# Optimization experiments

Hardware: AMD Instinct MI355X
Metric: run time of the kernel (lower is better)

## Reference

```python
import jax, jax.numpy as jnp
import numpy as np

B, S, D = 2, 2048, 768
H = 12
HD = D // H  # head_dim = 64
WINDOW = 128
NEG = -1e9


def setup_inputs() -> dict:
    key = jax.random.key(0)
    k1, k2, k3 = jax.random.split(key, 3)
    x = jax.random.normal(k1, (B, S, D), dtype=jnp.float32)
    padding_mask = jnp.ones((B, S), dtype=jnp.float32)
    Wqkv = jax.random.normal(k2, (D, 3 * D), dtype=jnp.float32) * (1.0 / np.sqrt(D))
    Wo = jax.random.normal(k3, (D, D), dtype=jnp.float32) * (1.0 / np.sqrt(D))
    return {"x": x, "padding_mask": padding_mask, "Wqkv": Wqkv, "Wo": Wo}


def reference(x, padding_mask, Wqkv, Wo):
    b, s = x.shape[0], x.shape[1]
    qkv = x @ Wqkv  # [b, s, 3D]
    qkv = qkv.reshape(b, s, 3, H, HD)
    q = qkv[:, :, 0]  # [b, s, H, HD]
    k = qkv[:, :, 1]
    v = qkv[:, :, 2]
    # scores: [b, H, s, s]
    scores = jnp.einsum("bqhd,bkhd->bhqk", q, k) / jnp.sqrt(jnp.asarray(HD, x.dtype))
    # sliding-window additive mask
    idx = jnp.arange(s)
    sw_mask = (jnp.abs(idx[:, None] - idx[None, :]) <= WINDOW // 2).astype(jnp.float32)
    scores = scores + (1.0 - sw_mask)[None, None, :, :] * NEG
    # padding mask over keys
    scores = scores + (1.0 - padding_mask)[:, None, None, :] * NEG
    attn = jax.nn.softmax(scores, axis=-1)
    out = jnp.einsum("bhqk,bkhd->bqhd", attn, v).reshape(b, s, D)
    return out @ Wo
```

## Files before the change

### kernel.cpp

```cpp
#include <hip/hip_runtime.h>
#include <stdint.h>

typedef short bf16x8 __attribute__((ext_vector_type(8)));
typedef float f32x4 __attribute__((ext_vector_type(4)));

#define SEQ_ 2048
#define DM_ 768
#define NH_ 12

__device__ __forceinline__ unsigned short f2bf(float f) {
  unsigned int u = __float_as_uint(f);
  u += 0x7fffu + ((u >> 16) & 1u);
  return (unsigned short)(u >> 16);
}

__device__ __forceinline__ void load_lds16(const unsigned short* g, unsigned short* l) {
  __builtin_amdgcn_global_load_lds((__attribute__((address_space(1))) void*)g,
                                   (__attribute__((address_space(3))) void*)l, 16, 0, 0);
}

__device__ __forceinline__ void transpose_body(const float* __restrict__ src,
                                               unsigned short* __restrict__ dst,
                                               int R, int C, int bx, int by,
                                               float (*t)[65]) {
  int c0 = bx << 6, r0 = by << 6;
  int tid = threadIdx.x;
#pragma unroll
  for (int i = 0; i < 4; i++) {
    int e = (i * 256 + tid) * 4;
    int r = e >> 6, c = e & 63;
    float4 v = *(const float4*)(src + (size_t)(r0 + r) * C + c0 + c);
    t[r][c] = v.x; t[r][c + 1] = v.y; t[r][c + 2] = v.z; t[r][c + 3] = v.w;
  }
  __syncthreads();
#pragma unroll
  for (int i = 0; i < 4; i++) {
    int e = (i * 256 + tid) * 4;
    int r = e >> 6, c = e & 63;
    unsigned short o4[4];
#pragma unroll
    for (int j = 0; j < 4; j++) o4[j] = f2bf(t[c + j][r]);
    *(uint2*)(dst + (size_t)(c0 + r) * R + r0 + c) = *(const uint2*)o4;
  }
}

__global__ __launch_bounds__(256) void prep(const float* __restrict__ x,
                                            const float* __restrict__ Wqkv,
                                            const float* __restrict__ Wo,
                                            unsigned short* __restrict__ xb,
                                            unsigned short* __restrict__ wqkvt,
                                            unsigned short* __restrict__ wot) {
  __shared__ float t[64][65];
  int blk = blockIdx.x;
  if (blk < 3072) {
    int i = (blk * 256 + threadIdx.x) * 4;
    float4 v = *(const float4*)(x + i);
    unsigned short o[4] = {f2bf(v.x), f2bf(v.y), f2bf(v.z), f2bf(v.w)};
    *(uint2*)(xb + i) = *(const uint2*)o;
  } else if (blk < 3072 + 432) {
    int idx = blk - 3072;
    transpose_body(Wqkv, wqkvt, DM_, 3 * DM_, idx % 36, idx / 36, t);
  } else {
    int idx = blk - 3504;
    transpose_body(Wo, wot, DM_, DM_, idx % 12, idx / 12, t);
  }
}

__device__ __forceinline__ void gemm_mainloop(const unsigned short* __restrict__ A,
                                              const unsigned short* __restrict__ Bt,
                                              int m0, int n0,
                                              unsigned short* As, unsigned short* Bs,
                                              f32x4 acc[4][4]) {
  const int K = 768;
  int tid = threadIdx.x, wv = tid >> 6, ln = tid & 63, quad = ln >> 4, lrow = ln & 15;
  const unsigned short* a0 = A + (size_t)(m0 + (tid >> 2)) * K + (tid & 3) * 8;
  const unsigned short* a1 = a0 + (size_t)64 * K;
  const unsigned short* b0 = Bt + (size_t)(n0 + (tid >> 2)) * K + (tid & 3) * 8;
  const unsigned short* b1 = b0 + (size_t)64 * K;
  int mw = (wv >> 1) << 6, nw = (wv & 1) << 6;
  for (int kt = 0; kt < K; kt += 32) {
    load_lds16(a0 + kt, As + tid * 8);
    load_lds16(a1 + kt, As + (256 + tid) * 8);
    load_lds16(b0 + kt, Bs + tid * 8);
    load_lds16(b1 + kt, Bs + (256 + tid) * 8);
    __syncthreads();
    bf16x8 af[4], bfr[4];
#pragma unroll
    for (int i = 0; i < 4; i++)
      af[i] = *(const bf16x8*)(As + (mw + i * 16 + lrow) * 32 + quad * 8);
#pragma unroll
    for (int j = 0; j < 4; j++)
      bfr[j] = *(const bf16x8*)(Bs + (nw + j * 16 + lrow) * 32 + quad * 8);
#pragma unroll
    for (int i = 0; i < 4; i++)
#pragma unroll
      for (int j = 0; j < 4; j++)
        acc[i][j] = __builtin_amdgcn_mfma_f32_16x16x32_bf16(af[i], bfr[j], acc[i][j], 0, 0, 0);
    __syncthreads();
  }
}

__global__ __launch_bounds__(256, 3) void gemm_qkv(const unsigned short* __restrict__ A,
                                                   const unsigned short* __restrict__ Bt,
                                                   unsigned short* __restrict__ Qb,
                                                   unsigned short* __restrict__ Kb,
                                                   unsigned short* __restrict__ Vtb) {
  __shared__ unsigned short smem[2 * 128 * 32];
  unsigned short* As = smem;
  unsigned short* Bs = smem + 128 * 32;
  f32x4 acc[4][4];
  f32x4 z = {0.f, 0.f, 0.f, 0.f};
#pragma unroll
  for (int i = 0; i < 4; i++)
#pragma unroll
    for (int j = 0; j < 4; j++) acc[i][j] = z;
  int m0 = blockIdx.x << 7, n0 = blockIdx.y << 7;
  gemm_mainloop(A, Bt, m0, n0, As, Bs, acc);
  int tid = threadIdx.x, wv = tid >> 6, ln = tid & 63, quad = ln >> 4, lrow = ln & 15;
  int mw_l = (wv >> 1) << 6, nw_l = (wv & 1) << 6;
  int bb = m0 >> 11;
  int which = n0 / DM_;
  int nrem0 = n0 - which * DM_;
  if (which < 2) {
    unsigned short* dstp = which == 0 ? Qb : Kb;
#pragma unroll
    for (int j = 0; j < 4; j++) {
      int nb = nrem0 + nw_l + j * 16;
      int h = nb >> 6, hdb = (nb & 63) + lrow;
      size_t hoff = (size_t)(bb * NH_ + h) << 11;
#pragma unroll
      for (int i = 0; i < 4; i++)
#pragma unroll
        for (int r = 0; r < 4; r++) {
          int s = (m0 + mw_l + i * 16 + quad * 4 + r) & (SEQ_ - 1);
          dstp[((hoff + s) << 6) + hdb] = f2bf(acc[i][j][r]);
        }
    }
  } else {
    const int LSTR = 136;
    int hdl2 = ((wv & 1) << 4) + lrow;
    int hds = tid >> 3, s0 = (tid & 7) << 4;
    int hd_in_block = ((hds & 16) << 2) + (hds & 15);
#pragma unroll
    for (int j = 0; j < 4; j++) {
      __syncthreads();
#pragma unroll
      for (int i = 0; i < 4; i++)
#pragma unroll
        for (int r = 0; r < 4; r++) {
          int sl = mw_l + i * 16 + quad * 4 + r;
          smem[hdl2 * LSTR + sl] = f2bf(acc[i][j][r]);
        }
      __syncthreads();
      int nb = nrem0 + hd_in_block + j * 16;
      int h = nb >> 6, hdh = nb & 63;
      uint4 p0 = *(const uint4*)&smem[hds * LSTR + s0];
      uint4 p1 = *(const uint4*)&smem[hds * LSTR + s0 + 8];
      size_t vbase = (size_t)(((bb * NH_ + h) << 6) + hdh) * SEQ_ + (m0 & (SEQ_ - 1)) + s0;
      *(uint4*)(Vtb + vbase) = p0;
      *(uint4*)(Vtb + vbase + 8) = p1;
    }
  }
}

__global__ __launch_bounds__(256, 3) void gemm_out(const unsigned short* __restrict__ A,
                                                   const unsigned short* __restrict__ Bt,
                                                   float* __restrict__ out) {
  const int K = 768;
  __shared__ unsigned short As[64 * 32];
  __shared__ unsigned short Bs[128 * 32];
  f32x4 acc[4][2];
  f32x4 z = {0.f, 0.f, 0.f, 0.f};
#pragma unroll
  for (int i = 0; i < 4; i++)
#pragma unroll
    for (int j = 0; j < 2; j++) acc[i][j] = z;
  int m0 = blockIdx.x << 6, n0 = blockIdx.y << 7;
  int tid = threadIdx.x, wv = tid >> 6, ln = tid & 63, quad = ln >> 4, lrow = ln & 15;
  const unsigned short* a0 = A + (size_t)(m0 + (tid >> 2)) * K + (tid & 3) * 8;
  const unsigned short* b0 = Bt + (size_t)(n0 + (tid >> 2)) * K + (tid & 3) * 8;
  const unsigned short* b1 = b0 + (size_t)64 * K;
  int nw = wv << 5;
  for (int kt = 0; kt < K; kt += 32) {
    load_lds16(a0 + kt, As + tid * 8);
    load_lds16(b0 + kt, Bs + tid * 8);
    load_lds16(b1 + kt, Bs + (256 + tid) * 8);
    __syncthreads();
    bf16x8 af[4], bfr[2];
#pragma unroll
    for (int i = 0; i < 4; i++)
      af[i] = *(const bf16x8*)(As + (i * 16 + lrow) * 32 + quad * 8);
#pragma unroll
    for (int j = 0; j < 2; j++)
      bfr[j] = *(const bf16x8*)(Bs + (nw + j * 16 + lrow) * 32 + quad * 8);
#pragma unroll
    for (int i = 0; i < 4; i++)
#pragma unroll
      for (int j = 0; j < 2; j++)
        acc[i][j] = __builtin_amdgcn_mfma_f32_16x16x32_bf16(af[i], bfr[j], acc[i][j], 0, 0, 0);
    __syncthreads();
  }
#pragma unroll
  for (int i = 0; i < 4; i++)
#pragma unroll
    for (int j = 0; j < 2; j++)
#pragma unroll
      for (int r = 0; r < 4; r++)
        out[(size_t)(m0 + i * 16 + quad * 4 + r) * DM_ + n0 + nw + j * 16 + lrow] = acc[i][j][r];
}

__global__ __launch_bounds__(256, 3) void attn_kernel(const unsigned short* __restrict__ Qb,
                                                      const unsigned short* __restrict__ Kb,
                                                      const unsigned short* __restrict__ Vtb,
                                                      const float* __restrict__ pmask,
                                                      unsigned short* __restrict__ Obf) {
  __shared__ unsigned short Ps[4][16 * 168];
  int blk = blockIdx.x;
  int tile = blk & 31, bh = blk >> 5;
  int b = bh / NH_, h = bh % NH_;
  int q0 = tile << 6;
  int kstart = q0 - 64;
  int tid = threadIdx.x, wv = tid >> 6, ln = tid & 63, quad = ln >> 4, lrow = ln & 15;
  int kb = wv << 4;
  int qw = q0 + (wv << 4);

  const unsigned short* Qg = Qb + ((size_t)bh << 11) * 64;
  const unsigned short* Kg = Kb + ((size_t)bh << 11) * 64;
  const unsigned short* Vg = Vtb + ((size_t)bh << 6) * SEQ_;

  bf16x8 qf0 = *(const bf16x8*)(Qg + (qw + lrow) * 64 + quad * 8);
  bf16x8 qf1 = *(const bf16x8*)(Qg + (qw + lrow) * 64 + 32 + quad * 8);

  float sc[9][4];
#pragma unroll
  for (int t = 0; t < 9; t++) {
    int kg = kstart + kb + t * 16 + lrow;
    int kgc = kg < 0 ? 0 : (kg > SEQ_ - 1 ? SEQ_ - 1 : kg);
    bf16x8 kf0 = *(const bf16x8*)(Kg + (size_t)kgc * 64 + quad * 8);
    bf16x8 kf1 = *(const bf16x8*)(Kg + (size_t)kgc * 64 + 32 + quad * 8);
    f32x4 c = {0.f, 0.f, 0.f, 0.f};
    c = __builtin_amdgcn_mfma_f32_16x16x32_bf16(qf0, kf0, c, 0, 0, 0);
    c = __builtin_amdgcn_mfma_f32_16x16x32_bf16(qf1, kf1, c, 0, 0, 0);
    float mneg = -1e30f;
    if (kg >= 0 && kg < SEQ_) {
      if (pmask[(b << 11) + kg] != 0.0f) mneg = 0.0f;
    }
#pragma unroll
    for (int r = 0; r < 4; r++) {
      int qg = qw + quad * 4 + r;
      int d = qg - kg;
      float wneg = (d >= -64 && d <= 64) ? 0.0f : -1e30f;
      sc[t][r] = c[r] * 0.125f + mneg + wneg;
    }
  }
  float inv[4];
#pragma unroll
  for (int r = 0; r < 4; r++) {
    float mx = sc[0][r];
#pragma unroll
    for (int t = 1; t < 9; t++) mx = fmaxf(mx, sc[t][r]);
    mx = fmaxf(mx, __shfl_xor(mx, 1));
    mx = fmaxf(mx, __shfl_xor(mx, 2));
    mx = fmaxf(mx, __shfl_xor(mx, 4));
    mx = fmaxf(mx, __shfl_xor(mx, 8));
    float s = 0.f;
#pragma unroll
    for (int t = 0; t < 9; t++) {
      sc[t][r] = __expf(sc[t][r] - mx);
      s += sc[t][r];
    }
    s += __shfl_xor(s, 1);
    s += __shfl_xor(s, 2);
    s += __shfl_xor(s, 4);
    s += __shfl_xor(s, 8);
    inv[r] = 1.0f / s;
  }
  unsigned short* Pw = &Ps[wv][0];
#pragma unroll
  for (int t = 0; t < 9; t++)
#pragma unroll
    for (int r = 0; r < 4; r++)
      Pw[(quad * 4 + r) * 168 + t * 16 + lrow] = f2bf(sc[t][r] * inv[r]);
  {
    int row = ln >> 2, c0 = 144 + (ln & 3) * 4;
    uint2 zz; zz.x = 0; zz.y = 0;
    *(uint2*)(Pw + row * 168 + c0) = zz;
  }
  __syncthreads();
  f32x4 o[4];
  f32x4 z = {0.f, 0.f, 0.f, 0.f};
#pragma unroll
  for (int tt = 0; tt < 4; tt++) o[tt] = z;
#pragma unroll
  for (int ks = 0; ks < 5; ks++) {
    bf16x8 pf = *(const bf16x8*)(Pw + lrow * 168 + ks * 32 + quad * 8);
    int kg = kstart + kb + ks * 32 + quad * 8;
    int kgc = kg < 0 ? 0 : (kg > SEQ_ - 8 ? SEQ_ - 8 : kg);
#pragma unroll
    for (int tt = 0; tt < 4; tt++) {
      bf16x8 vf = *(const bf16x8*)(Vg + (size_t)(tt * 16 + lrow) * SEQ_ + kgc);
      o[tt] = __builtin_amdgcn_mfma_f32_16x16x32_bf16(pf, vf, o[tt], 0, 0, 0);
    }
  }
#pragma unroll
  for (int tt = 0; tt < 4; tt++)
#pragma unroll
    for (int r = 0; r < 4; r++) {
      int s_ = qw + quad * 4 + r;
      Obf[((size_t)(b << 11) + s_) * DM_ + h * 64 + tt * 16 + lrow] = f2bf(o[tt][r]);
    }
}

extern "C" void kernel_launch(void* const* d_in, const int* in_sizes, int n_in,
                              void* d_out, int out_size, void* d_ws, size_t ws_size,
                              hipStream_t stream) {
  const float* x = (const float*)d_in[0];
  const float* pmask = (const float*)d_in[1];
  const float* Wqkv = (const float*)d_in[2];
  const float* Wo = (const float*)d_in[3];
  float* out = (float*)d_out;
  char* ws = (char*)d_ws;

  unsigned short* xb    = (unsigned short*)(ws + 0);
  unsigned short* wqkvt = (unsigned short*)(ws + 6291456);
  unsigned short* wot   = (unsigned short*)(ws + 9830400);
  unsigned short* Qb    = (unsigned short*)(ws + 11010048);
  unsigned short* Kb    = (unsigned short*)(ws + 17301504);
  unsigned short* Vtb   = (unsigned short*)(ws + 23592960);
  unsigned short* attn_bf = xb;

  prep<<<3648, 256, 0, stream>>>(x, Wqkv, Wo, xb, wqkvt, wot);
  gemm_qkv<<<dim3(32, 18), 256, 0, stream>>>(xb, wqkvt, Qb, Kb, Vtb);
  attn_kernel<<<768, 256, 0, stream>>>(Qb, Kb, Vtb, pmask, attn_bf);
  gemm_out<<<dim3(64, 6), 256, 0, stream>>>(attn_bf, wot, out);
}
```

Baseline: 134.6 us.

## Double GEMM K-step to 64 with XOR-swizzled LDS and retile output GEMM

```diff
diff --git a/kernel.cpp b/kernel.cpp
--- a/kernel.cpp
+++ b/kernel.cpp
@@ -73,29 +73,34 @@
                                               f32x4 acc[4][4]) {
   const int K = 768;
   int tid = threadIdx.x, wv = tid >> 6, ln = tid & 63, quad = ln >> 4, lrow = ln & 15;
-  const unsigned short* a0 = A + (size_t)(m0 + (tid >> 2)) * K + (tid & 3) * 8;
-  const unsigned short* a1 = a0 + (size_t)64 * K;
-  const unsigned short* b0 = Bt + (size_t)(n0 + (tid >> 2)) * K + (tid & 3) * 8;
-  const unsigned short* b1 = b0 + (size_t)64 * K;
+  int row = tid >> 3;
+  int col8 = (tid & 7) ^ (row & 7);
+  const unsigned short* a0 = A + (size_t)(m0 + row) * K + col8 * 8;
+  const unsigned short* b0 = Bt + (size_t)(n0 + row) * K + col8 * 8;
   int mw = (wv >> 1) << 6, nw = (wv & 1) << 6;
-  for (int kt = 0; kt < K; kt += 32) {
-    load_lds16(a0 + kt, As + tid * 8);
-    load_lds16(a1 + kt, As + (256 + tid) * 8);
-    load_lds16(b0 + kt, Bs + tid * 8);
-    load_lds16(b1 + kt, Bs + (256 + tid) * 8);
+  int sw = (lrow & 7);
+  for (int kt = 0; kt < K; kt += 64) {
+#pragma unroll
+    for (int st = 0; st < 4; st++) {
+      load_lds16(a0 + (size_t)(st * 32) * K + kt, As + (st * 256 + tid) * 8);
+      load_lds16(b0 + (size_t)(st * 32) * K + kt, Bs + (st * 256 + tid) * 8);
+    }
     __syncthreads();
-    bf16x8 af[4], bfr[4];
-#pragma unroll
-    for (int i = 0; i < 4; i++)
-      af[i] = *(const bf16x8*)(As + (mw + i * 16 + lrow) * 32 + quad * 8);
-#pragma unroll
-    for (int j = 0; j < 4; j++)
-      bfr[j] = *(const bf16x8*)(Bs + (nw + j * 16 + lrow) * 32 + quad * 8);
-#pragma unroll
-    for (int i = 0; i < 4; i++)
+#pragma unroll
+    for (int ks = 0; ks < 2; ks++) {
+      bf16x8 af[4], bfr[4];
+#pragma unroll
+      for (int i = 0; i < 4; i++)
+        af[i] = *(const bf16x8*)(As + (mw + i * 16 + lrow) * 64 + (((ks * 4 + quad) ^ sw) << 3));
 #pragma unroll
       for (int j = 0; j < 4; j++)
-        acc[i][j] = __builtin_amdgcn_mfma_f32_16x16x32_bf16(af[i], bfr[j], acc[i][j], 0, 0, 0);
+        bfr[j] = *(const bf16x8*)(Bs + (nw + j * 16 + lrow) * 64 + (((ks * 4 + quad) ^ sw) << 3));
+#pragma unroll
+      for (int i = 0; i < 4; i++)
+#pragma unroll
+        for (int j = 0; j < 4; j++)
+          acc[i][j] = __builtin_amdgcn_mfma_f32_16x16x32_bf16(af[i], bfr[j], acc[i][j], 0, 0, 0);
+    }
     __syncthreads();
   }
 }
@@ -105,9 +110,9 @@
                                                    unsigned short* __restrict__ Qb,
                                                    unsigned short* __restrict__ Kb,
                                                    unsigned short* __restrict__ Vtb) {
-  __shared__ unsigned short smem[2 * 128 * 32];
+  __shared__ unsigned short smem[2 * 128 * 64];
   unsigned short* As = smem;
-  unsigned short* Bs = smem + 128 * 32;
+  unsigned short* Bs = smem + 128 * 64;
   f32x4 acc[4][4];
   f32x4 z = {0.f, 0.f, 0.f, 0.f};
 #pragma unroll
@@ -167,46 +172,54 @@
                                                    const unsigned short* __restrict__ Bt,
                                                    float* __restrict__ out) {
   const int K = 768;
-  __shared__ unsigned short As[64 * 32];
-  __shared__ unsigned short Bs[128 * 32];
-  f32x4 acc[4][2];
+  __shared__ unsigned short As[128 * 64];
+  __shared__ unsigned short Bs[96 * 64];
+  f32x4 acc[4][3];
   f32x4 z = {0.f, 0.f, 0.f, 0.f};
 #pragma unroll
   for (int i = 0; i < 4; i++)
 #pragma unroll
-    for (int j = 0; j < 2; j++) acc[i][j] = z;
-  int m0 = blockIdx.x << 6, n0 = blockIdx.y << 7;
+    for (int j = 0; j < 3; j++) acc[i][j] = z;
+  int m0 = blockIdx.x << 7, n0 = blockIdx.y * 96;
   int tid = threadIdx.x, wv = tid >> 6, ln = tid & 63, quad = ln >> 4, lrow = ln & 15;
-  const unsigned short* a0 = A + (size_t)(m0 + (tid >> 2)) * K + (tid & 3) * 8;
-  const unsigned short* b0 = Bt + (size_t)(n0 + (tid >> 2)) * K + (tid & 3) * 8;
-  const unsigned short* b1 = b0 + (size_t)64 * K;
-  int nw = wv << 5;
-  for (int kt = 0; kt < K; kt += 32) {
-    load_lds16(a0 + kt, As + tid * 8);
-    load_lds16(b0 + kt, Bs + tid * 8);
-    load_lds16(b1 + kt, Bs + (256 + tid) * 8);
+  int row = tid >> 3;
+  int col8 = (tid & 7) ^ (row & 7);
+  const unsigned short* a0 = A + (size_t)(m0 + row) * K + col8 * 8;
+  const unsigned short* b0 = Bt + (size_t)(n0 + row) * K + col8 * 8;
+  int mw = (wv >> 1) << 6, nw = (wv & 1) * 48;
+  int sw = (lrow & 7);
+  for (int kt = 0; kt < K; kt += 64) {
+#pragma unroll
+    for (int st = 0; st < 4; st++)
+      load_lds16(a0 + (size_t)(st * 32) * K + kt, As + (st * 256 + tid) * 8);
+#pragma unroll
+    for (int st = 0; st < 3; st++)
+      load_lds16(b0 + (size_t)(st * 32) * K + kt, Bs + (st * 256 + tid) * 8);
     __syncthreads();
-    bf16x8 af[4], bfr[2];
-#pragma unroll
-    for (int i = 0; i < 4; i++)
-      af[i] = *(const bf16x8*)(As + (i * 16 + lrow) * 32 + quad * 8);
-#pragma unroll
-    for (int j = 0; j < 2; j++)
-      bfr[j] = *(const bf16x8*)(Bs + (nw + j * 16 + lrow) * 32 + quad * 8);
-#pragma unroll
-    for (int i = 0; i < 4; i++)
-#pragma unroll
-      for (int j = 0; j < 2; j++)
-        acc[i][j] = __builtin_amdgcn_mfma_f32_16x16x32_bf16(af[i], bfr[j], acc[i][j], 0, 0, 0);
+#pragma unroll
+    for (int ks = 0; ks < 2; ks++) {
+      bf16x8 af[4], bfr[3];
+#pragma unroll
+      for (int i = 0; i < 4; i++)
+        af[i] = *(const bf16x8*)(As + (mw + i * 16 + lrow) * 64 + (((ks * 4 + quad) ^ sw) << 3));
+#pragma unroll
+      for (int j = 0; j < 3; j++)
+        bfr[j] = *(const bf16x8*)(Bs + (nw + j * 16 + lrow) * 64 + (((ks * 4 + quad) ^ sw) << 3));
+#pragma unroll
+      for (int i = 0; i < 4; i++)
+#pragma unroll
+        for (int j = 0; j < 3; j++)
+          acc[i][j] = __builtin_amdgcn_mfma_f32_16x16x32_bf16(af[i], bfr[j], acc[i][j], 0, 0, 0);
+    }
     __syncthreads();
   }
 #pragma unroll
   for (int i = 0; i < 4; i++)
 #pragma unroll
-    for (int j = 0; j < 2; j++)
+    for (int j = 0; j < 3; j++)
 #pragma unroll
       for (int r = 0; r < 4; r++)
-        out[(size_t)(m0 + i * 16 + quad * 4 + r) * DM_ + n0 + nw + j * 16 + lrow] = acc[i][j][r];
+        out[(size_t)(m0 + mw + i * 16 + quad * 4 + r) * DM_ + n0 + nw + j * 16 + lrow] = acc[i][j][r];
 }
 
 __global__ __launch_bounds__(256, 3) void attn_kernel(const unsigned short* __restrict__ Qb,
@@ -332,5 +345,5 @@
   prep<<<3648, 256, 0, stream>>>(x, Wqkv, Wo, xb, wqkvt, wot);
   gemm_qkv<<<dim3(32, 18), 256, 0, stream>>>(xb, wqkvt, Qb, Kb, Vtb);
   attn_kernel<<<768, 256, 0, stream>>>(Qb, Kb, Vtb, pmask, attn_bf);
-  gemm_out<<<dim3(64, 6), 256, 0, stream>>>(attn_bf, wot, out);
-}
+  gemm_out<<<dim3(32, 8), 256, 0, stream>>>(attn_bf, wot, out);
+}
```

Result: faster. 128.8 us (-4.3%).
